# Performance work log

Hardware: AMD Instinct MI355X
Metric: run time of the kernel (lower is better)

The kernel has to match this reference:

```python
import jax, jax.numpy as jnp
import numpy as np
import math

DIM = 4096
N_HEADS = 32
HEAD_DIM = DIM // N_HEADS  # 128


def setup_inputs() -> dict:
    key = jax.random.key(0)
    ks = jax.random.split(key, 10)
    B, S, C = 2, 1024, 2048
    x = jax.random.normal(ks[0], (B, S, DIM), dtype=jnp.float32)
    freqs_cis = jax.random.normal(ks[1], (S, HEAD_DIM // 2), dtype=jnp.float32)
    mask = jnp.zeros((1, 1, S, C), dtype=jnp.float32)
    input_idexes = jnp.arange(S, dtype=jnp.int64) if jax.config.jax_enable_x64 else jnp.arange(S, dtype=jnp.int32)
    cache_k = jax.random.normal(ks[2], (B, C, N_HEADS, HEAD_DIM), dtype=jnp.float32) * 0.1
    cache_v = jax.random.normal(ks[3], (B, C, N_HEADS, HEAD_DIM), dtype=jnp.float32) * 0.1
    # Linear weights in torch layout [out_features, in_features], y = x @ W.T
    wq = jax.random.normal(ks[4], (DIM, DIM), dtype=jnp.float32) * 0.02
    wk = jax.random.normal(ks[5], (DIM, DIM), dtype=jnp.float32) * 0.02
    wv = jax.random.normal(ks[6], (DIM, DIM), dtype=jnp.float32) * 0.02
    wo = jax.random.normal(ks[7], (DIM, DIM), dtype=jnp.float32) * 0.02
    return {"x": x, "freqs_cis": freqs_cis, "mask": mask, "input_idexes": input_idexes,
            "cache_k": cache_k, "cache_v": cache_v, "wq": wq, "wk": wk, "wv": wv, "wo": wo}


def reference(x, freqs_cis, mask, input_idexes, cache_k, cache_v, wq, wk, wv, wo):
    B, S, D = x.shape
    H, hd = N_HEADS, HEAD_DIM
    # projections (torch Linear: x @ W.T)
    xq = jnp.einsum('bsd,ed->bse', x, wq).reshape(B, S, H, hd)
    # xk/xv are computed in the original forward but never used (cache-only attention)
    xk = jnp.einsum('bsd,ed->bse', x, wk).reshape(B, S, H, hd)  # noqa: F841
    xv = jnp.einsum('bsd,ed->bse', x, wv).reshape(B, S, H, hd)  # noqa: F841
    q = xq.transpose(0, 2, 1, 3)                 # [B,H,S,hd]
    keys = cache_k.transpose(0, 2, 1, 3)         # [B,H,C,hd]
    values = cache_v.transpose(0, 2, 1, 3)       # [B,H,C,hd]
    scores = jnp.einsum('bhse,bhce->bhsc', q, keys) / math.sqrt(hd)
    scores = scores + mask
    attn = jax.nn.softmax(scores.astype(jnp.float32), axis=-1).astype(q.dtype)
    out = jnp.einsum('bhsc,bhce->bhse', attn, values)  # [B,H,S,hd]
    out = out.transpose(0, 2, 1, 3).reshape(B, S, H * hd)
    return jnp.einsum('bse,de->bsd', out, wo)
```

## Files before the change

### kernel.cpp

```cpp
#include <hip/hip_runtime.h>
#include <hip/hip_bf16.h>
#include <stdint.h>


#define DIM   4096
#define NH    32
#define HD    128
#define BB    2
#define SS    1024
#define CC    2048

typedef __bf16 bf16x8 __attribute__((ext_vector_type(8)));
typedef float  f32x4  __attribute__((ext_vector_type(4)));

__device__ __forceinline__ unsigned short f2bf(float f) {
  union { __hip_bfloat16 h; unsigned short u; } cv;
  cv.h = __float2bfloat16(f);
  return cv.u;
}

__device__ __forceinline__ void gl_lds16(const void* g, void* l) {
  __builtin_amdgcn_global_load_lds(
      (__attribute__((address_space(1))) void*)(uintptr_t)(g),
      (__attribute__((address_space(3))) void*)(l), 16, 0, 0);
}

__global__ void conv_f32_bf16(const float* __restrict__ in, unsigned short* __restrict__ out, int n4) {
  int i = blockIdx.x * blockDim.x + threadIdx.x;
  int stride = gridDim.x * blockDim.x;
  for (; i < n4; i += stride) {
    float4 v = reinterpret_cast<const float4*>(in)[i];
    ushort4 o;
    o.x = f2bf(v.x); o.y = f2bf(v.y); o.z = f2bf(v.z); o.w = f2bf(v.w);
    reinterpret_cast<ushort4*>(out)[i] = o;
  }
}

__global__ __launch_bounds__(256) void prep_a(
    const float* __restrict__ x,  unsigned short* __restrict__ xbf,
    const float* __restrict__ wq, unsigned short* __restrict__ wbf)
{
  const int b = blockIdx.x, t = threadIdx.x;
  const float* in; unsigned short* out; int base, nthr, n4;
  if (b < 1024) { in = x;  out = xbf; base = b;        nthr = 1024 * 256; n4 = BB * SS * DIM / 4; }
  else          { in = wq; out = wbf; base = b - 1024; nthr = 2048 * 256; n4 = DIM * DIM / 4; }
  for (int i = base * 256 + t; i < n4; i += nthr) {
    float4 v = reinterpret_cast<const float4*>(in)[i];
    ushort4 o;
    o.x = f2bf(v.x); o.y = f2bf(v.y); o.z = f2bf(v.z); o.w = f2bf(v.w);
    reinterpret_cast<ushort4*>(out)[i] = o;
  }
}

__global__ __launch_bounds__(256) void prep_b(
    const float* __restrict__ ck,  unsigned short* __restrict__ kbf,
    const float* __restrict__ cv,  unsigned short* __restrict__ vtbf,
    const float* __restrict__ mask, int* __restrict__ flags)
{
  const int b = blockIdx.x, t = threadIdx.x;

  if (b < 2048) {
    const int total4 = BB * NH * CC * HD / 4;
    for (int i = b * 256 + t; i < total4; i += 2048 * 256) {
      size_t o = (size_t)i * 4;
      int d  = (int)(o & (HD - 1));
      size_t r = o >> 7;
      int c  = (int)(r & (CC - 1));
      int bh = (int)(r >> 11);
      int hh = bh & (NH - 1), bb = bh >> 5;
      float4 v = *reinterpret_cast<const float4*>(ck + ((size_t)(bb * CC + c) * NH + hh) * HD + d);
      ushort4 u; u.x = f2bf(v.x); u.y = f2bf(v.y); u.z = f2bf(v.z); u.w = f2bf(v.w);
      *reinterpret_cast<ushort4*>(kbf + o) = u;
    }
  } else if (b < 6144) {
    __shared__ float tile[64][65];
    const int e  = b - 2048;
    const int ct = e & 31, rest = e >> 5;
    const int dt = rest & 1, bh = rest >> 1;
    const int hh = bh & (NH - 1), bb = bh >> 5;
    const int c0 = ct * 64, d0 = dt * 64;
    const int tx = t & 63, ty = t >> 6;
#pragma unroll
    for (int i = 0; i < 16; ++i) {
      int cl = ty + i * 4;
      tile[cl][tx] = cv[((size_t)(bb * CC + c0 + cl) * NH + hh) * HD + d0 + tx];
    }
    __syncthreads();
    const int c4 = (t & 15) * 4, dr = t >> 4;
#pragma unroll
    for (int i = 0; i < 4; ++i) {
      int dl = dr + i * 16;
      ushort4 o;
      o.x = f2bf(tile[c4 + 0][dl]); o.y = f2bf(tile[c4 + 1][dl]);
      o.z = f2bf(tile[c4 + 2][dl]); o.w = f2bf(tile[c4 + 3][dl]);
      *reinterpret_cast<ushort4*>(&vtbf[((size_t)bh * HD + d0 + dl) * CC + c0 + c4]) = o;
    }
  } else {
    __shared__ int s[4];
    const int e  = b - 6144;
    const int qt = e >> 5, ct = e & 31;
    const int w = t >> 6;
    const float4* m4 = (const float4*)mask;
    int nz = 0;
#pragma unroll
    for (int i = 0; i < 8; ++i) {
      int idx = i * 256 + t;
      int row = idx >> 4, c4 = idx & 15;
      float4 v = m4[(size_t)(qt * 128 + row) * (CC / 4) + ct * 16 + c4];
      nz |= (v.x != 0.f) | (v.y != 0.f) | (v.z != 0.f) | (v.w != 0.f);
    }
    int wa = (int)__any(nz);
    if ((t & 63) == 0) s[w] = wa;
    __syncthreads();
    if (t == 0) flags[qt * 32 + ct] = s[0] | s[1] | s[2] | s[3];
  }
}

template <int OUT_BF16>
__global__ __launch_bounds__(256, 2) void gemm_bt(
    const unsigned short* __restrict__ A,
    const unsigned short* __restrict__ Bw,
    void* __restrict__ Cout,
    int M, int N, int K, float scale)
{
  __shared__ __align__(16) unsigned short As[128 * 32];
  __shared__ __align__(16) unsigned short Bs[128 * 32];
  const int t = threadIdx.x;
  const int w = t >> 6, lane = t & 63;
  const int wr = w >> 1, wc = w & 1;
  const int bm0 = blockIdx.y * 128, bn0 = blockIdx.x * 128;

  const unsigned short* aSrc = A  + (size_t)(bm0 + (t >> 2)) * K + (t & 3) * 8;
  const unsigned short* bSrc = Bw + (size_t)(bn0 + (t >> 2)) * K + (t & 3) * 8;
  char* aDst = (char*)As + w * 1024;
  char* bDst = (char*)Bs + w * 1024;
  const size_t half = (size_t)64 * K;

  f32x4 acc[4][4];
#pragma unroll
  for (int m = 0; m < 4; ++m)
#pragma unroll
    for (int n = 0; n < 4; ++n) acc[m][n] = (f32x4){0.f, 0.f, 0.f, 0.f};

  for (int k0 = 0; k0 < K; k0 += 32) {
    gl_lds16(aSrc,        aDst);
    gl_lds16(aSrc + half, aDst + 4096);
    gl_lds16(bSrc,        bDst);
    gl_lds16(bSrc + half, bDst + 4096);
    aSrc += 32; bSrc += 32;
    __syncthreads();

    bf16x8 af[4], bf[4];
#pragma unroll
    for (int m = 0; m < 4; ++m)
      af[m] = *(const bf16x8*)&As[(wr * 64 + m * 16 + (lane & 15)) * 32 + (lane >> 4) * 8];
#pragma unroll
    for (int n = 0; n < 4; ++n)
      bf[n] = *(const bf16x8*)&Bs[(wc * 64 + n * 16 + (lane & 15)) * 32 + (lane >> 4) * 8];
#pragma unroll
    for (int m = 0; m < 4; ++m)
#pragma unroll
      for (int n = 0; n < 4; ++n)
        acc[m][n] = __builtin_amdgcn_mfma_f32_16x16x32_bf16(af[m], bf[n], acc[m][n], 0, 0, 0);
    __syncthreads();
  }

  const int r0 = (lane >> 4) * 4, cl = lane & 15;
#pragma unroll
  for (int m = 0; m < 4; ++m) {
#pragma unroll
    for (int n = 0; n < 4; ++n) {
      int row = bm0 + wr * 64 + m * 16 + r0;
      int col = bn0 + wc * 64 + n * 16 + cl;
#pragma unroll
      for (int r = 0; r < 4; ++r) {
        float v = acc[m][n][r] * scale;
        if (OUT_BF16) ((unsigned short*)Cout)[(size_t)(row + r) * N + col] = f2bf(v);
        else          ((float*)Cout)[(size_t)(row + r) * N + col] = v;
      }
    }
  }
}

__global__ __launch_bounds__(256, 2) void attn_fwd(
    const unsigned short* __restrict__ Qb,
    const unsigned short* __restrict__ Kb,
    const unsigned short* __restrict__ Vtb,
    const float* __restrict__ mask,
    const int* __restrict__ Mf,
    unsigned short* __restrict__ Ob)
{
  __shared__ __align__(16) unsigned short Ks[2][64 * 128];
  __shared__ __align__(16) unsigned short Vs[2][64 * 128];
  __shared__ __align__(16) unsigned short Ps[4][32 * 64];

  const int t = threadIdx.x, w = t >> 6, lane = t & 63;
  const int lg = (blockIdx.x & 7) * 64 + (blockIdx.x >> 3);
  const int qt = lg & 7, bh = lg >> 3;
  const int hh = bh & (NH - 1), bb = bh >> 5;
  const int q0 = qt * 128;
  const int l15 = lane & 15, g = lane >> 4;
  const int rb4 = g * 4;

  bf16x8 qf[2][4];
#pragma unroll
  for (int rf = 0; rf < 2; ++rf) {
    const unsigned short* qp = Qb + ((size_t)(bb * SS + q0 + w * 32 + rf * 16 + l15)) * DIM
                               + hh * HD + g * 8;
#pragma unroll
    for (int kk = 0; kk < 4; ++kk)
      qf[rf][kk] = *(const bf16x8*)(qp + kk * 32);
  }

  const unsigned short* kSrc = Kb + ((size_t)bh * CC + (t >> 4)) * HD
                               + (((t & 15) ^ ((t >> 4) & 7)) * 8);
  const unsigned short* vSrc = Vtb + ((size_t)bh * HD + (t >> 3)) * CC
                               + (((t & 7) ^ ((t >> 3) & 7)) * 8);

  f32x4 acc_o[2][8];
#pragma unroll
  for (int rf = 0; rf < 2; ++rf)
#pragma unroll
    for (int i = 0; i < 8; ++i) acc_o[rf][i] = (f32x4){0.f, 0.f, 0.f, 0.f};
  float m_run[2][4], l_run[2][4];
#pragma unroll
  for (int rf = 0; rf < 2; ++rf)
#pragma unroll
    for (int r = 0; r < 4; ++r) { m_run[rf][r] = -1e30f; l_run[rf][r] = 0.f; }

  const int swz = (lane & 7) << 3;
  const float LOG2E = 1.4426950408889634f;

  int mflag = Mf[qt * 32];
  {
    char* kd = (char*)Ks[0] + w * 1024;
    char* vd = (char*)Vs[0] + w * 1024;
#pragma unroll
    for (int i = 0; i < 4; ++i) {
      gl_lds16(kSrc + (size_t)(i * 16) * HD, kd + i * 4096);
      gl_lds16(vSrc + (size_t)i * 32 * CC,   vd + i * 4096);
    }
  }
  __syncthreads();

  int cur = 0;
  for (int c0 = 0; c0 < CC; c0 += 64) {
    const int ct = c0 >> 6;
    int nextFlag = (ct < 31) ? Mf[qt * 32 + ct + 1] : 0;

    float mk[2][4][4];
    if (mflag) {
#pragma unroll
      for (int rf = 0; rf < 2; ++rf)
#pragma unroll
        for (int nf = 0; nf < 4; ++nf)
#pragma unroll
          for (int r = 0; r < 4; ++r)
            mk[rf][nf][r] = mask[(size_t)(q0 + w * 32 + rf * 16 + rb4 + r) * CC
                                 + c0 + nf * 16 + l15];
      __builtin_amdgcn_sched_barrier(0);
    }

    if (c0 + 64 < CC) {
      char* kd = (char*)Ks[cur ^ 1] + w * 1024;
      char* vd = (char*)Vs[cur ^ 1] + w * 1024;
#pragma unroll
      for (int i = 0; i < 4; ++i) {
        gl_lds16(kSrc + (size_t)(c0 + 64 + i * 16) * HD, kd + i * 4096);
        gl_lds16(vSrc + (size_t)i * 32 * CC + c0 + 64,   vd + i * 4096);
      }
    }
    __builtin_amdgcn_sched_barrier(0);

    f32x4 sc[2][4];
#pragma unroll
    for (int rf = 0; rf < 2; ++rf)
#pragma unroll
      for (int nf = 0; nf < 4; ++nf) sc[rf][nf] = (f32x4){0.f, 0.f, 0.f, 0.f};
    __builtin_amdgcn_s_setprio(1);
#pragma unroll
    for (int kk = 0; kk < 4; ++kk) {
#pragma unroll
      for (int nf = 0; nf < 4; ++nf) {
        bf16x8 kf = *(const bf16x8*)&Ks[cur][((nf * 16 + l15) * 128 + kk * 32 + g * 8) ^ swz];
        sc[0][nf] = __builtin_amdgcn_mfma_f32_16x16x32_bf16(qf[0][kk], kf, sc[0][nf], 0, 0, 0);
        sc[1][nf] = __builtin_amdgcn_mfma_f32_16x16x32_bf16(qf[1][kk], kf, sc[1][nf], 0, 0, 0);
      }
    }
    __builtin_amdgcn_s_setprio(0);

    if (mflag) {
#pragma unroll
      for (int rf = 0; rf < 2; ++rf)
#pragma unroll
        for (int nf = 0; nf < 4; ++nf)
#pragma unroll
          for (int r = 0; r < 4; ++r)
            sc[rf][nf][r] = fmaf(mk[rf][nf][r], LOG2E, sc[rf][nf][r]);
    }

#pragma unroll
    for (int rf = 0; rf < 2; ++rf) {
      int ok = 1;
      float pm[4];
#pragma unroll
      for (int r = 0; r < 4; ++r) {
        pm[r] = fmaxf(fmaxf(sc[rf][0][r], sc[rf][1][r]), fmaxf(sc[rf][2][r], sc[rf][3][r]));
        ok = ok && (pm[r] <= m_run[rf][r] + 8.0f);
      }
      if (!__all(ok)) {
#pragma unroll
        for (int r = 0; r < 4; ++r) {
          float mx = pm[r];
#pragma unroll
          for (int d = 1; d < 16; d <<= 1)
            mx = fmaxf(mx, __shfl_xor(mx, d));
          float mn = fmaxf(m_run[rf][r], mx);
          float corr = __builtin_amdgcn_exp2f(m_run[rf][r] - mn);
          m_run[rf][r] = mn;
          l_run[rf][r] *= corr;
#pragma unroll
          for (int nd = 0; nd < 8; ++nd) acc_o[rf][nd][r] *= corr;
        }
      }

#pragma unroll
      for (int r = 0; r < 4; ++r) {
        int rw = rf * 16 + rb4 + r;
        int rsw = (rw & 7) << 3;
#pragma unroll
        for (int nf = 0; nf < 4; ++nf) {
          float p = __builtin_amdgcn_exp2f(sc[rf][nf][r] - m_run[rf][r]);
          l_run[rf][r] += p;
          Ps[w][rw * 64 + ((nf * 16 + l15) ^ rsw)] = f2bf(p);
        }
      }
    }

    __builtin_amdgcn_s_setprio(1);
#pragma unroll
    for (int kk = 0; kk < 2; ++kk) {
      bf16x8 pf0 = *(const bf16x8*)&Ps[w][((0 * 16 + l15) * 64 + kk * 32 + g * 8) ^ swz];
      bf16x8 pf1 = *(const bf16x8*)&Ps[w][((1 * 16 + l15) * 64 + kk * 32 + g * 8) ^ swz];
#pragma unroll
      for (int nd = 0; nd < 8; ++nd) {
        bf16x8 vf = *(const bf16x8*)&Vs[cur][((nd * 16 + l15) * 64 + kk * 32 + g * 8) ^ swz];
        acc_o[0][nd] = __builtin_amdgcn_mfma_f32_16x16x32_bf16(pf0, vf, acc_o[0][nd], 0, 0, 0);
        acc_o[1][nd] = __builtin_amdgcn_mfma_f32_16x16x32_bf16(pf1, vf, acc_o[1][nd], 0, 0, 0);
      }
    }
    __builtin_amdgcn_s_setprio(0);
    __syncthreads();
    cur ^= 1;
    mflag = nextFlag;
  }

#pragma unroll
  for (int rf = 0; rf < 2; ++rf) {
#pragma unroll
    for (int r = 0; r < 4; ++r)
#pragma unroll
      for (int d = 1; d < 16; d <<= 1)
        l_run[rf][r] += __shfl_xor(l_run[rf][r], d);

#pragma unroll
    for (int nd = 0; nd < 8; ++nd)
#pragma unroll
      for (int r = 0; r < 4; ++r) {
        float v = acc_o[rf][nd][r] / l_run[rf][r];
        int row = q0 + w * 32 + rf * 16 + rb4 + r;
        Ob[(size_t)(bb * SS + row) * DIM + hh * HD + nd * 16 + l15] = f2bf(v);
      }
  }
}

extern "C" void kernel_launch(void* const* d_in, const int* in_sizes, int n_in,
                              void* d_out, int out_size, void* d_ws, size_t ws_size,
                              hipStream_t stream) {
  const float* x       = (const float*)d_in[0];
  const float* mask    = (const float*)d_in[2];
  const float* cache_k = (const float*)d_in[4];
  const float* cache_v = (const float*)d_in[5];
  const float* wq      = (const float*)d_in[6];
  const float* wo      = (const float*)d_in[9];
  float* out = (float*)d_out;

  char* ws = (char*)d_ws;
  unsigned short* Wbf  = (unsigned short*)(ws);
  unsigned short* xbf  = (unsigned short*)(ws + 33554432);
  unsigned short* qbf  = (unsigned short*)(ws + 33554432 + 16777216);
  unsigned short* kbf  = (unsigned short*)(ws + 33554432 + 2 * 16777216);
  unsigned short* vtbf = (unsigned short*)(ws + 2 * 33554432 + 2 * 16777216);
  int* mflags = (int*)d_out;

  dim3 gg(DIM / 128, (BB * SS) / 128);
  prep_a<<<3072, 256, 0, stream>>>(x, xbf, wq, Wbf);
  gemm_bt<1><<<gg, 256, 0, stream>>>(xbf, Wbf, qbf, BB * SS, DIM, DIM, 0.12751744682f);
  prep_b<<<6400, 256, 0, stream>>>(cache_k, kbf, cache_v, vtbf, mask, mflags);
  attn_fwd<<<BB * NH * 8, 256, 0, stream>>>(qbf, kbf, vtbf, mask, mflags, xbf);
  conv_f32_bf16<<<2048, 256, 0, stream>>>(wo, Wbf, DIM * DIM / 4);
  gemm_bt<0><<<gg, 256, 0, stream>>>(xbf, Wbf, out, BB * SS, DIM, DIM, 1.0f);
}
```

Baseline: 355.6 us.

## Fuse Q projection GEMM into attention kernel prologue

Each attention block now computes its own 128x128 Q tile (one head, 128 query rows) directly from bf16 x and Wq, using a simple single-buffered MFMA loop. It stages the result in shared memory and loads the Q fragments from there. This removes the separate Q GEMM launch and the write and read of Q through global memory. The cost is that the fused GEMM loop syncs twice per k-step with no double buffering, which may run slower than the tuned standalone GEMM. The attention output buffer moves to qbf, and LDS is merged into one shared array.

```diff
diff --git a/kernel.cpp b/kernel.cpp
--- a/kernel.cpp
+++ b/kernel.cpp
@@ -182,17 +182,16 @@
   }
 }
 
-__global__ __launch_bounds__(256, 2) void attn_fwd(
-    const unsigned short* __restrict__ Qb,
+__global__ __launch_bounds__(256, 2) void fused_qattn(
+    const unsigned short* __restrict__ Ax,
+    const unsigned short* __restrict__ Wq,
     const unsigned short* __restrict__ Kb,
     const unsigned short* __restrict__ Vtb,
     const float* __restrict__ mask,
     const int* __restrict__ Mf,
     unsigned short* __restrict__ Ob)
 {
-  __shared__ __align__(16) unsigned short Ks[2][64 * 128];
-  __shared__ __align__(16) unsigned short Vs[2][64 * 128];
-  __shared__ __align__(16) unsigned short Ps[4][32 * 64];
+  __shared__ __align__(16) unsigned short SM[40960];
 
   const int t = threadIdx.x, w = t >> 6, lane = t & 63;
   const int lg = (blockIdx.x & 7) * 64 + (blockIdx.x >> 3);
@@ -201,16 +200,78 @@
   const int q0 = qt * 128;
   const int l15 = lane & 15, g = lane >> 4;
   const int rb4 = g * 4;
-
+  const int wr = w >> 1, wc = w & 1;
+
+  const int bm0 = bb * SS + q0;
+  const int bn0 = hh * HD;
+  {
+    unsigned short* As = SM;
+    unsigned short* Bs = SM + 4096;
+    const unsigned short* aSrc = Ax + (size_t)(bm0 + (t >> 2)) * DIM + (t & 3) * 8;
+    const unsigned short* bSrc = Wq + (size_t)(bn0 + (t >> 2)) * DIM + (t & 3) * 8;
+    char* aDst = (char*)As + w * 1024;
+    char* bDst = (char*)Bs + w * 1024;
+    const size_t half = (size_t)64 * DIM;
+
+    f32x4 acc[4][4];
+#pragma unroll
+    for (int m = 0; m < 4; ++m)
+#pragma unroll
+      for (int n = 0; n < 4; ++n) acc[m][n] = (f32x4){0.f, 0.f, 0.f, 0.f};
+
+    for (int k0 = 0; k0 < DIM; k0 += 32) {
+      gl_lds16(aSrc,        aDst);
+      gl_lds16(aSrc + half, aDst + 4096);
+      gl_lds16(bSrc,        bDst);
+      gl_lds16(bSrc + half, bDst + 4096);
+      aSrc += 32; bSrc += 32;
+      __syncthreads();
+
+      bf16x8 af[4], bf[4];
+#pragma unroll
+      for (int m = 0; m < 4; ++m)
+        af[m] = *(const bf16x8*)&As[(wr * 64 + m * 16 + l15) * 32 + g * 8];
+#pragma unroll
+      for (int n = 0; n < 4; ++n)
+        bf[n] = *(const bf16x8*)&Bs[(wc * 64 + n * 16 + l15) * 32 + g * 8];
+#pragma unroll
+      for (int m = 0; m < 4; ++m)
+#pragma unroll
+        for (int n = 0; n < 4; ++n)
+          acc[m][n] = __builtin_amdgcn_mfma_f32_16x16x32_bf16(af[m], bf[n], acc[m][n], 0, 0, 0);
+      __syncthreads();
+    }
+
+    const float qscale = 0.12751744682f;
+    const int r0 = g * 4;
+#pragma unroll
+    for (int m = 0; m < 4; ++m) {
+#pragma unroll
+      for (int n = 0; n < 4; ++n) {
+        int rl = wr * 64 + m * 16 + r0;
+        int cl2 = wc * 64 + n * 16 + l15;
+#pragma unroll
+        for (int r = 0; r < 4; ++r) {
+          int row = rl + r;
+          SM[(row * 128 + cl2) ^ ((row & 7) << 3)] = f2bf(acc[m][n][r] * qscale);
+        }
+      }
+    }
+  }
+  __syncthreads();
+
+  const int swz = (lane & 7) << 3;
   bf16x8 qf[2][4];
 #pragma unroll
   for (int rf = 0; rf < 2; ++rf) {
-    const unsigned short* qp = Qb + ((size_t)(bb * SS + q0 + w * 32 + rf * 16 + l15)) * DIM
-                               + hh * HD + g * 8;
+    int row = w * 32 + rf * 16 + l15;
 #pragma unroll
     for (int kk = 0; kk < 4; ++kk)
-      qf[rf][kk] = *(const bf16x8*)(qp + kk * 32);
-  }
+      qf[rf][kk] = *(const bf16x8*)&SM[(row * 128 + kk * 32 + g * 8) ^ swz];
+  }
+  __syncthreads();
+
+  unsigned short* PsW = SM + 32768 + w * 2048;
 
   const unsigned short* kSrc = Kb + ((size_t)bh * CC + (t >> 4)) * HD
                                + (((t & 15) ^ ((t >> 4) & 7)) * 8);
@@ -228,13 +289,12 @@
 #pragma unroll
     for (int r = 0; r < 4; ++r) { m_run[rf][r] = -1e30f; l_run[rf][r] = 0.f; }
 
-  const int swz = (lane & 7) << 3;
   const float LOG2E = 1.4426950408889634f;
 
   int mflag = Mf[qt * 32];
   {
-    char* kd = (char*)Ks[0] + w * 1024;
-    char* vd = (char*)Vs[0] + w * 1024;
+    char* kd = (char*)(SM)         + w * 1024;
+    char* vd = (char*)(SM + 16384) + w * 1024;
 #pragma unroll
     for (int i = 0; i < 4; ++i) {
       gl_lds16(kSrc + (size_t)(i * 16) * HD, kd + i * 4096);
@@ -247,6 +307,8 @@
   for (int c0 = 0; c0 < CC; c0 += 64) {
     const int ct = c0 >> 6;
     int nextFlag = (ct < 31) ? Mf[qt * 32 + ct + 1] : 0;
+    unsigned short* KsC = SM + cur * 8192;
+    unsigned short* VsC = SM + 16384 + cur * 8192;
 
     float mk[2][4][4];
     if (mflag) {
@@ -262,8 +324,8 @@
     }
 
     if (c0 + 64 < CC) {
-      char* kd = (char*)Ks[cur ^ 1] + w * 1024;
-      char* vd = (char*)Vs[cur ^ 1] + w * 1024;
+      char* kd = (char*)(SM + (cur ^ 1) * 8192)         + w * 1024;
+      char* vd = (char*)(SM + 16384 + (cur ^ 1) * 8192) + w * 1024;
 #pragma unroll
       for (int i = 0; i < 4; ++i) {
         gl_lds16(kSrc + (size_t)(c0 + 64 + i * 16) * HD, kd + i * 4096);
@@ -282,7 +344,7 @@
     for (int kk = 0; kk < 4; ++kk) {
 #pragma unroll
       for (int nf = 0; nf < 4; ++nf) {
-        bf16x8 kf = *(const bf16x8*)&Ks[cur][((nf * 16 + l15) * 128 + kk * 32 + g * 8) ^ swz];
+        bf16x8 kf = *(const bf16x8*)&KsC[((nf * 16 + l15) * 128 + kk * 32 + g * 8) ^ swz];
         sc[0][nf] = __builtin_amdgcn_mfma_f32_16x16x32_bf16(qf[0][kk], kf, sc[0][nf], 0, 0, 0);
         sc[1][nf] = __builtin_amdgcn_mfma_f32_16x16x32_bf16(qf[1][kk], kf, sc[1][nf], 0, 0, 0);
       }
@@ -332,7 +394,7 @@
         for (int nf = 0; nf < 4; ++nf) {
           float p = __builtin_amdgcn_exp2f(sc[rf][nf][r] - m_run[rf][r]);
           l_run[rf][r] += p;
-          Ps[w][rw * 64 + ((nf * 16 + l15) ^ rsw)] = f2bf(p);
+          PsW[rw * 64 + ((nf * 16 + l15) ^ rsw)] = f2bf(p);
         }
       }
     }
@@ -340,11 +402,11 @@
     __builtin_amdgcn_s_setprio(1);
 #pragma unroll
     for (int kk = 0; kk < 2; ++kk) {
-      bf16x8 pf0 = *(const bf16x8*)&Ps[w][((0 * 16 + l15) * 64 + kk * 32 + g * 8) ^ swz];
-      bf16x8 pf1 = *(const bf16x8*)&Ps[w][((1 * 16 + l15) * 64 + kk * 32 + g * 8) ^ swz];
+      bf16x8 pf0 = *(const bf16x8*)&PsW[((0 * 16 + l15) * 64 + kk * 32 + g * 8) ^ swz];
+      bf16x8 pf1 = *(const bf16x8*)&PsW[((1 * 16 + l15) * 64 + kk * 32 + g * 8) ^ swz];
 #pragma unroll
       for (int nd = 0; nd < 8; ++nd) {
-        bf16x8 vf = *(const bf16x8*)&Vs[cur][((nd * 16 + l15) * 64 + kk * 32 + g * 8) ^ swz];
+        bf16x8 vf = *(const bf16x8*)&VsC[((nd * 16 + l15) * 64 + kk * 32 + g * 8) ^ swz];
         acc_o[0][nd] = __builtin_amdgcn_mfma_f32_16x16x32_bf16(pf0, vf, acc_o[0][nd], 0, 0, 0);
         acc_o[1][nd] = __builtin_amdgcn_mfma_f32_16x16x32_bf16(pf1, vf, acc_o[1][nd], 0, 0, 0);
       }
@@ -393,11 +455,10 @@
   unsigned short* vtbf = (unsigned short*)(ws + 2 * 33554432 + 2 * 16777216);
   int* mflags = (int*)d_out;
 
+  prep_b<<<6400, 256, 0, stream>>>(cache_k, kbf, cache_v, vtbf, mask, mflags);
+  prep_a<<<3072, 256, 0, stream>>>(x, xbf, wq, Wbf);
+  fused_qattn<<<BB * NH * 8, 256, 0, stream>>>(xbf, Wbf, kbf, vtbf, mask, mflags, qbf);
+  conv_f32_bf16<<<2048, 256, 0, stream>>>(wo, Wbf, DIM * DIM / 4);
   dim3 gg(DIM / 128, (BB * SS) / 128);
-  prep_a<<<3072, 256, 0, stream>>>(x, xbf, wq, Wbf);
-  gemm_bt<1><<<gg, 256, 0, stream>>>(xbf, Wbf, qbf, BB * SS, DIM, DIM, 0.12751744682f);
-  prep_b<<<6400, 256, 0, stream>>>(cache_k, kbf, cache_v, vtbf, mask, mflags);
-  attn_fwd<<<BB * NH * 8, 256, 0, stream>>>(qbf, kbf, vtbf, mask, mflags, xbf);
-  conv_f32_bf16<<<2048, 256, 0, stream>>>(wo, Wbf, DIM * DIM / 4);
-  gemm_bt<0><<<gg, 256, 0, stream>>>(xbf, Wbf, out, BB * SS, DIM, DIM, 1.0f);
-}
+  gemm_bt<0><<<gg, 256, 0, stream>>>(qbf, Wbf, out, BB * SS, DIM, DIM, 1.0f);
+}
```

Measured after the change: 345.7 us, median of 2. -2.8%, faster.
